# Kernel tuning notes

Measured on AMD Instinct MI355X. Metric: run time of the kernel, lower is better.

## Reference

```python
import jax, jax.numpy as jnp
import numpy as np

HEADS = 16

def setup_inputs() -> dict:
    key = jax.random.key(0)
    ks = jax.random.split(key, 7)
    B, Lq, Lkv, D = 2, 1024, 2048, 1024
    return {
        "x_cond": jax.random.normal(ks[0], (B, Lkv, D), dtype=jnp.float32),
        "x_query": jax.random.normal(ks[1], (B, Lq, D), dtype=jnp.float32),
        "tok_emb": jax.random.normal(ks[2], (2, D), dtype=jnp.float32) * 0.02,
        "in_proj_w": jax.random.normal(ks[3], (3 * D, D), dtype=jnp.float32) * (1.0 / np.sqrt(D)),
        "in_proj_b": jax.random.normal(ks[4], (3 * D,), dtype=jnp.float32) * 0.02,
        "out_w": jax.random.normal(ks[5], (D, D), dtype=jnp.float32) * (1.0 / np.sqrt(D)),
        "out_b": jax.random.normal(ks[6], (D,), dtype=jnp.float32) * 0.02,
    }


def reference(x_cond, x_query, tok_emb, in_proj_w, in_proj_b, out_w, out_b):
    B, Lq, D = x_query.shape
    Lkv = x_cond.shape[1]
    H = HEADS
    hd = D // H
    # token-type embedding add: modality 0 -> condition, modality 1 -> query (last input)
    k_in = x_cond + tok_emb[0]    # [B, Lkv, D]
    q_in = x_query + tok_emb[1]   # [B, Lq, D]
    # packed in-projection (PyTorch MultiheadAttention layout: [3D, D])
    wq, wk, wv = jnp.split(in_proj_w, 3, axis=0)
    bq, bk, bv = jnp.split(in_proj_b, 3, axis=0)
    q = (q_in @ wq.T + bq).reshape(B, Lq, H, hd).transpose(0, 2, 1, 3)   # [B,H,Lq,hd]
    k = (k_in @ wk.T + bk).reshape(B, Lkv, H, hd).transpose(0, 2, 1, 3)  # [B,H,Lkv,hd]
    v = (k_in @ wv.T + bv).reshape(B, Lkv, H, hd).transpose(0, 2, 1, 3)  # [B,H,Lkv,hd]
    scale = 1.0 / jnp.sqrt(jnp.asarray(hd, dtype=q.dtype))
    scores = jnp.einsum("bhqd,bhkd->bhqk", q * scale, k)  # [B,H,Lq,Lkv]
    attn = jax.nn.softmax(scores, axis=-1)
    ctx = jnp.einsum("bhqk,bhkd->bhqd", attn, v)           # [B,H,Lq,hd]
    ctx = ctx.transpose(0, 2, 1, 3).reshape(B, Lq, D)
    fused_output = ctx @ out_w.T + out_b                    # [B,Lq,D]
    attn_weights = attn.mean(axis=1)                        # averaged over heads: [B,Lq,Lkv]
    return fused_output, attn_weights
```

## Files before the change

### kernel.cpp

```cpp
#include <hip/hip_runtime.h>
#include <hip/hip_bf16.h>
#include <cstddef>
#include <cstdint>


typedef float  f32x4  __attribute__((ext_vector_type(4)));
typedef short  bf16x8 __attribute__((ext_vector_type(8)));
typedef unsigned short u16x8 __attribute__((ext_vector_type(8)));
typedef __attribute__((address_space(1))) const void gvoid;
typedef __attribute__((address_space(3))) void lvoid;
#define GLD16(g, l) __builtin_amdgcn_global_load_lds((gvoid*)(g), (lvoid*)(l), 16, 0, 0)
#define WAIT_VM0()   asm volatile("s_waitcnt vmcnt(0)" ::: "memory")
#define WAIT_LGKM0() asm volatile("s_waitcnt lgkmcnt(0)" ::: "memory")
#define BAR() __builtin_amdgcn_s_barrier()
#define LOG2E 1.4426950408889634f

static __device__ __forceinline__ unsigned short f2bf(float f) {
    union { float f; unsigned u; } v; v.f = f;
    unsigned r = v.u + 0x7fff + ((v.u >> 16) & 1);
    return (unsigned short)(r >> 16);
}

__global__ __launch_bounds__(256)
void conv_bf16(const float* __restrict__ x, const float* __restrict__ tok,
               unsigned short* __restrict__ out, int n8)
{
    int i = blockIdx.x * 256 + threadIdx.x;
    if (i >= n8) return;
    const float4* src = (const float4*)x + (size_t)i * 2;
    float4 a = src[0], b = src[1];
    if (tok) {
        int col = (i * 8) & 1023;
        const float4* tp = (const float4*)(tok + col);
        float4 t0 = tp[0], t1 = tp[1];
        a.x += t0.x; a.y += t0.y; a.z += t0.z; a.w += t0.w;
        b.x += t1.x; b.y += t1.y; b.z += t1.z; b.w += t1.w;
    }
    u16x8 r;
    r[0] = f2bf(a.x); r[1] = f2bf(a.y); r[2] = f2bf(a.z); r[3] = f2bf(a.w);
    r[4] = f2bf(b.x); r[5] = f2bf(b.y); r[6] = f2bf(b.z); r[7] = f2bf(b.w);
    ((u16x8*)out)[i] = r;
}

__global__ __launch_bounds__(256)
void gemm_qkv(const unsigned short* __restrict__ Aq,
              const unsigned short* __restrict__ Ac,
              const unsigned short* __restrict__ W,
              const float* __restrict__ bias,
              unsigned short* __restrict__ Qh,
              unsigned short* __restrict__ Kh,
              unsigned short* __restrict__ Vh)
{
    __shared__ unsigned short As[128 * 64];
    __shared__ unsigned short Bs[128 * 64];
    const int t  = threadIdx.x;
    const int wv = t >> 6, ln = t & 63;
    const int wr = wv >> 1, wc = wv & 1;
    const int lr = ln & 15, lg = ln >> 4;
    const int y = blockIdx.y;

    const unsigned short* A; const unsigned short* Wp; const float* bs;
    unsigned short* Y; int Lshift, m0; float scale;
    if (y < 16)      { A = Aq; m0 = y * 128;        Wp = W;           bs = bias;        Y = Qh; Lshift = 10; scale = 0.125f; }
    else if (y < 48) { A = Ac; m0 = (y - 16) * 128; Wp = W + 1048576; bs = bias + 1024; Y = Kh; Lshift = 11; scale = 1.0f; }
    else             { A = Ac; m0 = (y - 48) * 128; Wp = W + 2097152; bs = bias + 2048; Y = Vh; Lshift = 11; scale = 1.0f; }
    const int n0 = blockIdx.x * 128;

    f32x4 acc[4][4] = {};

    for (int k0 = 0; k0 < 1024; k0 += 64) {
        __syncthreads();
#pragma unroll
        for (int ia = 0; ia < 4; ++ia) {
            int idx = ia * 256 + t;
            int row = idx >> 3, c = idx & 7;
            int sw = (c ^ (row & 7)) * 8;
            GLD16(A  + (size_t)(m0 + row) * 1024 + k0 + sw, As + idx * 8);
            GLD16(Wp + (size_t)(n0 + row) * 1024 + k0 + sw, Bs + idx * 8);
        }
        WAIT_VM0();
        __syncthreads();
#pragma unroll
        for (int ks = 0; ks < 2; ++ks) {
            bf16x8 af[4], bf[4];
#pragma unroll
            for (int i = 0; i < 4; ++i) {
                int rowA = wr * 64 + i * 16 + lr;
                af[i] = *(const bf16x8*)(As + rowA * 64 + (((ks * 4 + lg) ^ (rowA & 7)) * 8));
                int rowB = wc * 64 + i * 16 + lr;
                bf[i] = *(const bf16x8*)(Bs + rowB * 64 + (((ks * 4 + lg) ^ (rowB & 7)) * 8));
            }
#pragma unroll
            for (int i = 0; i < 4; ++i)
#pragma unroll
                for (int j = 0; j < 4; ++j)
                    acc[i][j] = __builtin_amdgcn_mfma_f32_16x16x32_bf16(af[i], bf[j], acc[i][j], 0, 0, 0);
        }
    }

#pragma unroll
    for (int i = 0; i < 4; ++i) {
        int rb = m0 + wr * 64 + i * 16 + lg * 4;
#pragma unroll
        for (int j = 0; j < 4; ++j) {
            int col = n0 + wc * 64 + j * 16 + lr;
            float bv = bs[col];
#pragma unroll
            for (int rr = 0; rr < 4; ++rr) {
                float v = (acc[i][j][rr] + bv) * scale;
                int r = rb + rr;
                int b = r >> Lshift, l = r & ((1 << Lshift) - 1);
                int hh = col >> 6, d = col & 63;
                Y[((((size_t)b * 16 + hh) << Lshift) + l) * 64 + d] = f2bf(v);
            }
        }
    }
}

__global__ __launch_bounds__(256)
void gemm_mfma(const unsigned short* __restrict__ A,
               const unsigned short* __restrict__ W,
               const float* __restrict__ bias,
               float* __restrict__ Y)
{
    __shared__ unsigned short As[128 * 64];
    __shared__ unsigned short Bs[128 * 64];
    const int t  = threadIdx.x;
    const int wv = t >> 6, ln = t & 63;
    const int wr = wv >> 1, wc = wv & 1;
    const int lr = ln & 15, lg = ln >> 4;
    const int m0 = blockIdx.y * 128, n0 = blockIdx.x * 128;

    f32x4 acc[4][4] = {};

    for (int k0 = 0; k0 < 1024; k0 += 64) {
        __syncthreads();
#pragma unroll
        for (int ia = 0; ia < 4; ++ia) {
            int idx = ia * 256 + t;
            int row = idx >> 3, c = idx & 7;
            int sw = (c ^ (row & 7)) * 8;
            GLD16(A + (size_t)(m0 + row) * 1024 + k0 + sw, As + idx * 8);
            GLD16(W + (size_t)(n0 + row) * 1024 + k0 + sw, Bs + idx * 8);
        }
        WAIT_VM0();
        __syncthreads();
#pragma unroll
        for (int ks = 0; ks < 2; ++ks) {
            bf16x8 af[4], bf[4];
#pragma unroll
            for (int i = 0; i < 4; ++i) {
                int rowA = wr * 64 + i * 16 + lr;
                af[i] = *(const bf16x8*)(As + rowA * 64 + (((ks * 4 + lg) ^ (rowA & 7)) * 8));
                int rowB = wc * 64 + i * 16 + lr;
                bf[i] = *(const bf16x8*)(Bs + rowB * 64 + (((ks * 4 + lg) ^ (rowB & 7)) * 8));
            }
#pragma unroll
            for (int i = 0; i < 4; ++i)
#pragma unroll
                for (int j = 0; j < 4; ++j)
                    acc[i][j] = __builtin_amdgcn_mfma_f32_16x16x32_bf16(af[i], bf[j], acc[i][j], 0, 0, 0);
        }
    }

#pragma unroll
    for (int i = 0; i < 4; ++i) {
        int rb = m0 + wr * 64 + i * 16 + lg * 4;
#pragma unroll
        for (int j = 0; j < 4; ++j) {
            int col = n0 + wc * 64 + j * 16 + lr;
            float bv = bias[col];
#pragma unroll
            for (int rr = 0; rr < 4; ++rr)
                Y[(size_t)(rb + rr) * 1024 + col] = acc[i][j][rr] + bv;
        }
    }
}

__global__ __launch_bounds__(256)
void transpose_v(const unsigned short* __restrict__ Vh, unsigned short* __restrict__ Vt)
{
    __shared__ unsigned short L[64 * 72];
    const int t = threadIdx.x;
    const int kt = blockIdx.x;
    const int bh = blockIdx.y;
    const unsigned short* src = Vh + ((size_t)bh * 2048 + kt * 64) * 64;
#pragma unroll
    for (int i = 0; i < 2; ++i) {
        int idx = i * 256 + t;
        int kv = idx >> 3, c = idx & 7;
        *(bf16x8*)(L + kv * 72 + c * 8) = *(const bf16x8*)(src + kv * 64 + c * 8);
    }
    __syncthreads();
#pragma unroll
    for (int i = 0; i < 2; ++i) {
        int idx = i * 256 + t;
        int d = idx >> 3, ck = idx & 7;
        u16x8 r;
#pragma unroll
        for (int j = 0; j < 8; ++j) r[j] = L[(ck * 8 + j) * 72 + d];
        *(u16x8*)(Vt + ((size_t)bh * 64 + d) * 2048 + kt * 64 + ck * 8) = r;
    }
}

__global__ __launch_bounds__(256)
void flash_fwd(const unsigned short* __restrict__ Q,
               const unsigned short* __restrict__ K,
               const unsigned short* __restrict__ Vt,
               unsigned short* __restrict__ ctx,
               float* __restrict__ m2Out, float* __restrict__ linvOut)
{
    __shared__ unsigned short Ks[2][4096];
    __shared__ unsigned short Vs[2][4096];
    __shared__ unsigned int   Ps32[64 * 36];
    const int t  = threadIdx.x;
    const int wv = t >> 6, ln = t & 63;
    const int lr = ln & 15, lg = ln >> 4;
    const int qt = blockIdx.x, h = blockIdx.y, b = blockIdx.z;
    const int bh = b * 16 + h;
    const int q0 = qt * 64;

    const int i0 = t, i1 = 256 + t;
    const int r0 = i0 >> 3, c0 = i0 & 7, sw0 = (c0 ^ (r0 & 7)) * 8;
    const int r1 = i1 >> 3, c1 = i1 & 7, sw1 = (c1 ^ (r1 & 7)) * 8;
    const int l0 = i0 * 8, l1 = i1 * 8;
    const int gk0 = r0 * 64 + sw0,   gk1 = r1 * 64 + sw1;
    const int gv0 = r0 * 2048 + sw0, gv1 = r1 * 2048 + sw1;

    int koff[4];
#pragma unroll
    for (int cf = 0; cf < 4; ++cf)
        koff[cf] = (cf * 16 + lr) * 64 + ((lg ^ (lr & 7)) * 8);
    const int pw32 = (wv * 16 + lr) * 36 + lg * 2;
    const int prH  = (wv * 16 + lr) * 72 + lg * 8;

    bf16x8 qf[2];
    {
        const unsigned short* qp = Q + ((size_t)bh * 1024 + q0 + wv * 16 + lr) * 64 + lg * 8;
        qf[0] = *(const bf16x8*)qp;
        qf[1] = *(const bf16x8*)(qp + 32);
    }

    f32x4 cacc[4] = {};
    float m2 = -1e30f, lsum = 0.f;

    const unsigned short* kp = K  + (size_t)bh * 2048 * 64;
    const unsigned short* vp = Vt + (size_t)bh * 64 * 2048;

    GLD16(kp + gk0, &Ks[0][l0]); GLD16(kp + gk1, &Ks[0][l1]);
    GLD16(vp + gv0, &Vs[0][l0]); GLD16(vp + gv1, &Vs[0][l1]);
    kp += 4096; vp += 64;
    WAIT_VM0();
    BAR();

    int cur = 0;
    for (int tile = 0; tile < 32; ++tile) {
        if (tile < 31) {
            GLD16(kp + gk0, &Ks[cur ^ 1][l0]); GLD16(kp + gk1, &Ks[cur ^ 1][l1]);
            GLD16(vp + gv0, &Vs[cur ^ 1][l0]); GLD16(vp + gv1, &Vs[cur ^ 1][l1]);
            kp += 4096; vp += 64;
        }

        f32x4 sacc[4] = {};
#pragma unroll
        for (int cf = 0; cf < 4; ++cf) {
            bf16x8 kf0 = *(const bf16x8*)(Ks[cur] + koff[cf]);
            sacc[cf] = __builtin_amdgcn_mfma_f32_16x16x32_bf16(kf0, qf[0], sacc[cf], 0, 0, 0);
            bf16x8 kf1 = *(const bf16x8*)(Ks[cur] + (koff[cf] ^ 32));
            sacc[cf] = __builtin_amdgcn_mfma_f32_16x16x32_bf16(kf1, qf[1], sacc[cf], 0, 0, 0);
        }

        float rm;
        {
            float a0 = fmaxf(fmaxf(sacc[0][0], sacc[0][1]), fmaxf(sacc[0][2], sacc[0][3]));
            float a1 = fmaxf(fmaxf(sacc[1][0], sacc[1][1]), fmaxf(sacc[1][2], sacc[1][3]));
            float a2 = fmaxf(fmaxf(sacc[2][0], sacc[2][1]), fmaxf(sacc[2][2], sacc[2][3]));
            float a3 = fmaxf(fmaxf(sacc[3][0], sacc[3][1]), fmaxf(sacc[3][2], sacc[3][3]));
            rm = fmaxf(fmaxf(a0, a1), fmaxf(a2, a3));
        }
        rm = fmaxf(rm, __shfl_xor(rm, 16, 64));
        rm = fmaxf(rm, __shfl_xor(rm, 32, 64));
        rm *= LOG2E;

        if (__any(rm > m2)) {
            float nm = fmaxf(m2, rm);
            float sc = exp2f(m2 - nm);
            m2 = nm;
            lsum *= sc;
            float scB[4];
#pragma unroll
            for (int rr = 0; rr < 4; ++rr)
                scB[rr] = __shfl(sc, (ln & 48) | (lg * 4 + rr), 64);
#pragma unroll
            for (int df = 0; df < 4; ++df)
#pragma unroll
                for (int rr = 0; rr < 4; ++rr) cacc[df][rr] *= scB[rr];
        }

        float p[4][4];
#pragma unroll
        for (int cf = 0; cf < 4; ++cf)
#pragma unroll
            for (int rr = 0; rr < 4; ++rr)
                p[cf][rr] = exp2f(fmaf(sacc[cf][rr], LOG2E, -m2));
#pragma unroll
        for (int cf = 0; cf < 4; ++cf) {
            Ps32[pw32 + cf * 8 + 0] = (unsigned)f2bf(p[cf][0]) | ((unsigned)f2bf(p[cf][1]) << 16);
            Ps32[pw32 + cf * 8 + 1] = (unsigned)f2bf(p[cf][2]) | ((unsigned)f2bf(p[cf][3]) << 16);
        }

        float rs;
        {
            float s0 = (p[0][0] + p[0][1]) + (p[0][2] + p[0][3]);
            float s1 = (p[1][0] + p[1][1]) + (p[1][2] + p[1][3]);
            float s2 = (p[2][0] + p[2][1]) + (p[2][2] + p[2][3]);
            float s3 = (p[3][0] + p[3][1]) + (p[3][2] + p[3][3]);
            rs = (s0 + s1) + (s2 + s3);
        }
        rs += __shfl_xor(rs, 16, 64);
        rs += __shfl_xor(rs, 32, 64);
        lsum += rs;

        WAIT_LGKM0();

#pragma unroll
        for (int kvs = 0; kvs < 2; ++kvs) {
            bf16x8 pf = *(const bf16x8*)((const unsigned short*)Ps32 + prH + kvs * 32);
#pragma unroll
            for (int df = 0; df < 4; ++df) {
                bf16x8 vf = *(const bf16x8*)(Vs[cur] + (koff[df] ^ (kvs * 32)));
                cacc[df] = __builtin_amdgcn_mfma_f32_16x16x32_bf16(pf, vf, cacc[df], 0, 0, 0);
            }
        }
        WAIT_VM0();
        BAR();
        cur ^= 1;
    }

    float inv = 1.f / lsum;
    float invB[4];
#pragma unroll
    for (int rr = 0; rr < 4; ++rr)
        invB[rr] = __shfl(inv, (ln & 48) | (lg * 4 + rr), 64);
#pragma unroll
    for (int df = 0; df < 4; ++df) {
#pragma unroll
        for (int rr = 0; rr < 4; ++rr) {
            int row = q0 + wv * 16 + lg * 4 + rr;
            int col = h * 64 + df * 16 + lr;
            ctx[((size_t)b * 1024 + row) * 1024 + col] = f2bf(cacc[df][rr] * invB[rr]);
        }
    }
    if (lg == 0) {
        size_t idx = (size_t)bh * 1024 + q0 + wv * 16 + lr;
        m2Out[idx]   = m2;
        linvOut[idx] = inv;
    }
}

__global__ __launch_bounds__(256)
void attn_mean_mfma(const unsigned short* __restrict__ Q,
                    const unsigned short* __restrict__ K,
                    const float* __restrict__ m2In, const float* __restrict__ linvIn,
                    float* __restrict__ attnOut)
{
    __shared__ unsigned short Ks[2][64 * 64];
    const int t  = threadIdx.x;
    const int wv = t >> 6, ln = t & 63;
    const int lr = ln & 15, lg = ln >> 4;
    const int kt = blockIdx.x, qt = blockIdx.y, b = blockIdx.z;
    const int q0 = qt * 64, kv0 = kt * 64;

    const int i0 = t, i1 = 256 + t;
    const int r0 = i0 >> 3, c0 = i0 & 7, sw0 = (c0 ^ (r0 & 7)) * 8;
    const int r1 = i1 >> 3, c1 = i1 & 7, sw1 = (c1 ^ (r1 & 7)) * 8;
    const int l0 = i0 * 8, l1 = i1 * 8;
    const int gk0 = r0 * 64 + sw0, gk1 = r1 * 64 + sw1;

    int koff[4];
#pragma unroll
    for (int cf = 0; cf < 4; ++cf)
        koff[cf] = (cf * 16 + lr) * 64 + ((lg ^ (lr & 7)) * 8);

    const unsigned short* kp = K + ((size_t)(b * 16) * 2048 + kv0) * 64;
    const unsigned short* qp = Q + ((size_t)(b * 16) * 1024 + q0 + wv * 16 + lr) * 64 + lg * 8;
    size_t ridx = (size_t)(b * 16) * 1024 + q0 + wv * 16 + lg * 4;

    float att[4][4] = {};

    GLD16(kp + gk0, &Ks[0][l0]); GLD16(kp + gk1, &Ks[0][l1]);
    kp += 131072;
    WAIT_VM0();
    BAR();

    int cur = 0;
    for (int h = 0; h < 16; ++h) {
        if (h < 15) {
            GLD16(kp + gk0, &Ks[cur ^ 1][l0]); GLD16(kp + gk1, &Ks[cur ^ 1][l1]);
            kp += 131072;
        }
        bf16x8 qf0 = *(const bf16x8*)qp;
        bf16x8 qf1 = *(const bf16x8*)(qp + 32);
        qp += 65536;
        float m2r[4], lir[4];
#pragma unroll
        for (int rr = 0; rr < 4; ++rr) {
            m2r[rr] = m2In[ridx + rr];
            lir[rr] = linvIn[ridx + rr];
        }
        ridx += 1024;

        f32x4 sacc[4] = {};
#pragma unroll
        for (int cf = 0; cf < 4; ++cf) {
            bf16x8 kf0 = *(const bf16x8*)(Ks[cur] + koff[cf]);
            sacc[cf] = __builtin_amdgcn_mfma_f32_16x16x32_bf16(qf0, kf0, sacc[cf], 0, 0, 0);
            bf16x8 kf1 = *(const bf16x8*)(Ks[cur] + (koff[cf] ^ 32));
            sacc[cf] = __builtin_amdgcn_mfma_f32_16x16x32_bf16(qf1, kf1, sacc[cf], 0, 0, 0);
        }
#pragma unroll
        for (int cf = 0; cf < 4; ++cf)
#pragma unroll
            for (int rr = 0; rr < 4; ++rr)
                att[cf][rr] += exp2f(sacc[cf][rr] * LOG2E - m2r[rr]) * lir[rr];

        WAIT_VM0();
        BAR();
        cur ^= 1;
    }

#pragma unroll
    for (int cf = 0; cf < 4; ++cf)
#pragma unroll
        for (int rr = 0; rr < 4; ++rr) {
            int row = q0 + wv * 16 + lg * 4 + rr;
            int col = kv0 + cf * 16 + lr;
            attnOut[((size_t)b * 1024 + row) * 2048 + col] = att[cf][rr] * 0.0625f;
        }
}

extern "C" void kernel_launch(void* const* d_in, const int* in_sizes, int n_in,
                              void* d_out, int out_size, void* d_ws, size_t ws_size,
                              hipStream_t stream)
{
    const float* x_cond  = (const float*)d_in[0];
    const float* x_query = (const float*)d_in[1];
    const float* tok     = (const float*)d_in[2];
    const float* w_in    = (const float*)d_in[3];
    const float* b_in    = (const float*)d_in[4];
    const float* w_out   = (const float*)d_in[5];
    const float* b_out   = (const float*)d_in[6];

    float* fused = (float*)d_out;
    float* attn  = (float*)d_out + 2097152;

    unsigned short* ws = (unsigned short*)d_ws;
    unsigned short* Aq   = ws;
    unsigned short* Ac   = Aq   + 2097152;
    unsigned short* Wb   = Ac   + 4194304;
    unsigned short* Qh   = Wb   + 4194304;
    unsigned short* Kh   = Qh   + 2097152;
    unsigned short* Vh   = Kh   + 4194304;
    unsigned short* Vt   = Vh   + 4194304;
    unsigned short* ctxb = Vt   + 4194304;
    float* m2b = (float*)(ctxb + 2097152);
    float* lib = m2b + 32768;

    conv_bf16<<<1024, 256, 0, stream>>>(x_query, tok + 1024, Aq, 262144);
    conv_bf16<<<2048, 256, 0, stream>>>(x_cond,  tok,        Ac, 524288);
    conv_bf16<<<1536, 256, 0, stream>>>(w_in,  nullptr, Wb,           393216);
    conv_bf16<<< 512, 256, 0, stream>>>(w_out, nullptr, Wb + 3145728, 131072);

    gemm_qkv<<<dim3(8, 80), 256, 0, stream>>>(Aq, Ac, Wb, b_in, Qh, Kh, Vh);

    transpose_v<<<dim3(32, 32), 256, 0, stream>>>(Vh, Vt);

    flash_fwd<<<dim3(16, 16, 2), 256, 0, stream>>>(Qh, Kh, Vt, ctxb, m2b, lib);
    attn_mean_mfma<<<dim3(32, 16, 2), 256, 0, stream>>>(Qh, Kh, m2b, lib, attn);

    gemm_mfma<<<dim3(8, 16), 256, 0, stream>>>(ctxb, Wb + 3145728, b_out, fused);
}
```

Baseline: 256.8 us.

## Split flash attention along KV into two chunks and merge partials

Flash attention now splits the 2048-key range into two 1024-key halves per block (split-K), doubling the grid from 512 to 1024 blocks to improve occupancy on the GPU. Each half writes unnormalized bf16 partial context plus row max and sum, and a new combine kernel rescales and merges them, producing the ctx, m2 and inverse-sum buffers. The P tile in LDS also switches to an XOR-swizzled layout without padding to avoid bank conflicts. Costs are an extra kernel launch, extra global traffic for the partials, and bf16 rounding of the unnormalized partials.

```diff
diff --git a/kernel.cpp b/kernel.cpp
--- a/kernel.cpp
+++ b/kernel.cpp
@@ -20,6 +20,9 @@
     unsigned r = v.u + 0x7fff + ((v.u >> 16) & 1);
     return (unsigned short)(r >> 16);
 }
+static __device__ __forceinline__ float bf2f(unsigned short u) {
+    union { unsigned u; float f; } v; v.u = (unsigned)u << 16; return v.f;
+}
 
 __global__ __launch_bounds__(256)
 void conv_bf16(const float* __restrict__ x, const float* __restrict__ tok,
@@ -207,17 +210,17 @@
 void flash_fwd(const unsigned short* __restrict__ Q,
                const unsigned short* __restrict__ K,
                const unsigned short* __restrict__ Vt,
-               unsigned short* __restrict__ ctx,
-               float* __restrict__ m2Out, float* __restrict__ linvOut)
+               unsigned short* __restrict__ pctx,
+               float* __restrict__ pm,
+               float* __restrict__ pl)
 {
     __shared__ unsigned short Ks[2][4096];
     __shared__ unsigned short Vs[2][4096];
-    __shared__ unsigned int   Ps32[64 * 36];
+    __shared__ unsigned int   Ps32[64 * 32];
     const int t  = threadIdx.x;
     const int wv = t >> 6, ln = t & 63;
     const int lr = ln & 15, lg = ln >> 4;
-    const int qt = blockIdx.x, h = blockIdx.y, b = blockIdx.z;
-    const int bh = b * 16 + h;
+    const int qt = blockIdx.x, ch = blockIdx.y, bh = blockIdx.z;
     const int q0 = qt * 64;
 
     const int i0 = t, i1 = 256 + t;
@@ -231,8 +234,10 @@
 #pragma unroll
     for (int cf = 0; cf < 4; ++cf)
         koff[cf] = (cf * 16 + lr) * 64 + ((lg ^ (lr & 7)) * 8);
-    const int pw32 = (wv * 16 + lr) * 36 + lg * 2;
-    const int prH  = (wv * 16 + lr) * 72 + lg * 8;
+    const int pwB = (wv * 16 + lr) * 32;
+    const int pxr = (lr & 7) * 4;
+    const int prq0 = (wv * 16 + lr) * 64 + ((lg ^ (lr & 7)) * 8);
+    const int prq1 = (wv * 16 + lr) * 64 + (((4 + lg) ^ (lr & 7)) * 8);
 
     bf16x8 qf[2];
     {
@@ -244,8 +249,8 @@
     f32x4 cacc[4] = {};
     float m2 = -1e30f, lsum = 0.f;
 
-    const unsigned short* kp = K  + (size_t)bh * 2048 * 64;
-    const unsigned short* vp = Vt + (size_t)bh * 64 * 2048;
+    const unsigned short* kp = K  + ((size_t)bh * 2048 + ch * 1024) * 64;
+    const unsigned short* vp = Vt + (size_t)bh * 64 * 2048 + ch * 1024;
 
     GLD16(kp + gk0, &Ks[0][l0]); GLD16(kp + gk1, &Ks[0][l1]);
     GLD16(vp + gv0, &Vs[0][l0]); GLD16(vp + gv1, &Vs[0][l1]);
@@ -254,8 +259,8 @@
     BAR();
 
     int cur = 0;
-    for (int tile = 0; tile < 32; ++tile) {
-        if (tile < 31) {
+    for (int tile = 0; tile < 16; ++tile) {
+        if (tile < 15) {
             GLD16(kp + gk0, &Ks[cur ^ 1][l0]); GLD16(kp + gk1, &Ks[cur ^ 1][l1]);
             GLD16(vp + gv0, &Vs[cur ^ 1][l0]); GLD16(vp + gv1, &Vs[cur ^ 1][l1]);
             kp += 4096; vp += 64;
@@ -305,8 +310,10 @@
                 p[cf][rr] = exp2f(fmaf(sacc[cf][rr], LOG2E, -m2));
 #pragma unroll
         for (int cf = 0; cf < 4; ++cf) {
-            Ps32[pw32 + cf * 8 + 0] = (unsigned)f2bf(p[cf][0]) | ((unsigned)f2bf(p[cf][1]) << 16);
-            Ps32[pw32 + cf * 8 + 1] = (unsigned)f2bf(p[cf][2]) | ((unsigned)f2bf(p[cf][3]) << 16);
+            Ps32[pwB + ((cf * 8 + lg * 2 + 0) ^ pxr)] =
+                (unsigned)f2bf(p[cf][0]) | ((unsigned)f2bf(p[cf][1]) << 16);
+            Ps32[pwB + ((cf * 8 + lg * 2 + 1) ^ pxr)] =
+                (unsigned)f2bf(p[cf][2]) | ((unsigned)f2bf(p[cf][3]) << 16);
         }
 
         float rs;
@@ -325,7 +332,7 @@
 
 #pragma unroll
         for (int kvs = 0; kvs < 2; ++kvs) {
-            bf16x8 pf = *(const bf16x8*)((const unsigned short*)Ps32 + prH + kvs * 32);
+            bf16x8 pf = *(const bf16x8*)((const unsigned short*)Ps32 + (kvs ? prq1 : prq0));
 #pragma unroll
             for (int df = 0; df < 4; ++df) {
                 bf16x8 vf = *(const bf16x8*)(Vs[cur] + (koff[df] ^ (kvs * 32)));
@@ -337,25 +344,44 @@
         cur ^= 1;
     }
 
-    float inv = 1.f / lsum;
-    float invB[4];
-#pragma unroll
-    for (int rr = 0; rr < 4; ++rr)
-        invB[rr] = __shfl(inv, (ln & 48) | (lg * 4 + rr), 64);
-#pragma unroll
-    for (int df = 0; df < 4; ++df) {
-#pragma unroll
-        for (int rr = 0; rr < 4; ++rr) {
-            int row = q0 + wv * 16 + lg * 4 + rr;
-            int col = h * 64 + df * 16 + lr;
-            ctx[((size_t)b * 1024 + row) * 1024 + col] = f2bf(cacc[df][rr] * invB[rr]);
-        }
-    }
+    size_t rbase = (size_t)bh * 1024 + q0 + wv * 16;
+    unsigned short* pc = pctx + ((size_t)ch * 32768 + rbase) * 64;
+#pragma unroll
+    for (int df = 0; df < 4; ++df)
+#pragma unroll
+        for (int rr = 0; rr < 4; ++rr)
+            pc[(lg * 4 + rr) * 64 + df * 16 + lr] = f2bf(cacc[df][rr]);
     if (lg == 0) {
-        size_t idx = (size_t)bh * 1024 + q0 + wv * 16 + lr;
-        m2Out[idx]   = m2;
-        linvOut[idx] = inv;
-    }
+        size_t idx = (size_t)ch * 32768 + rbase + lr;
+        pm[idx] = m2;
+        pl[idx] = lsum;
+    }
+}
+
+__global__ __launch_bounds__(256)
+void combine_flash(const unsigned short* __restrict__ pctx,
+                   const float* __restrict__ pm, const float* __restrict__ pl,
+                   unsigned short* __restrict__ ctxb,
+                   float* __restrict__ m2Out, float* __restrict__ linvOut)
+{
+    int gid = blockIdx.x * 256 + threadIdx.x;
+    int r = gid >> 3, dg = (gid & 7) * 8;
+    float m0 = pm[r], m1 = pm[32768 + r];
+    float l0 = pl[r], l1 = pl[32768 + r];
+    float M = fmaxf(m0, m1);
+    float s0 = exp2f(m0 - M), s1 = exp2f(m1 - M);
+    float L = fmaf(l0, s0, l1 * s1);
+    float linv = 1.f / L;
+    float f0 = s0 * linv, f1 = s1 * linv;
+    u16x8 a = *(const u16x8*)(pctx + (size_t)r * 64 + dg);
+    u16x8 b = *(const u16x8*)(pctx + (size_t)(32768 + r) * 64 + dg);
+    u16x8 o;
+#pragma unroll
+    for (int j = 0; j < 8; ++j)
+        o[j] = f2bf(fmaf(bf2f(a[j]), f0, bf2f(b[j]) * f1));
+    int bb = r >> 14, h = (r >> 10) & 15, q = r & 1023;
+    *(u16x8*)(ctxb + ((size_t)(bb * 1024) + q) * 1024 + h * 64 + dg) = o;
+    if (dg == 0) { m2Out[r] = M; linvOut[r] = linv; }
 }
 
 __global__ __launch_bounds__(256)
@@ -466,6 +492,10 @@
     float* m2b = (float*)(ctxb + 2097152);
     float* lib = m2b + 32768;
 
+    unsigned short* pctx = ws;
+    float* pmb = (float*)(ws + 4194304);
+    float* plb = pmb + 65536;
+
     conv_bf16<<<1024, 256, 0, stream>>>(x_query, tok + 1024, Aq, 262144);
     conv_bf16<<<2048, 256, 0, stream>>>(x_cond,  tok,        Ac, 524288);
     conv_bf16<<<1536, 256, 0, stream>>>(w_in,  nullptr, Wb,           393216);
@@ -475,7 +505,8 @@
 
     transpose_v<<<dim3(32, 32), 256, 0, stream>>>(Vh, Vt);
 
-    flash_fwd<<<dim3(16, 16, 2), 256, 0, stream>>>(Qh, Kh, Vt, ctxb, m2b, lib);
+    flash_fwd<<<dim3(16, 2, 32), 256, 0, stream>>>(Qh, Kh, Vt, pctx, pmb, plb);
+    combine_flash<<<1024, 256, 0, stream>>>(pctx, pmb, plb, ctxb, m2b, lib);
     attn_mean_mfma<<<dim3(32, 16, 2), 256, 0, stream>>>(Qh, Kh, m2b, lib, attn);
 
     gemm_mfma<<<dim3(8, 16), 256, 0, stream>>>(ctxb, Wb + 3145728, b_out, fused);
```

Result: faster. 250.5 us (-2.4%).
